# Optimization experiments

Hardware: AMD Instinct MI355X
Metric: run time of the kernel (lower is better)

## Reference

```python
import jax, jax.numpy as jnp
import numpy as np

D_MODEL = 1024
N_HEADS = 16
N_KV_HEADS = 4
HEAD_DIM = D_MODEL // N_HEADS  # 64
N_REP = N_HEADS // N_KV_HEADS  # 4
THETA = 10000.0
LOGIT_CAP = 30.0
EPS = 1e-6
SCALE = HEAD_DIM ** -0.5


def rmsnorm(x, w):
    return x * jax.lax.rsqrt(jnp.mean(x * x, axis=-1, keepdims=True) + EPS) * w


def rope_tables(seq_len, dtype):
    inv_freq = 1.0 / (THETA ** (jnp.arange(0, HEAD_DIM, 2, dtype=jnp.float32) / HEAD_DIM))
    t = jnp.arange(seq_len, dtype=jnp.float32)
    freqs = jnp.outer(t, inv_freq)                      # [S, hd/2]
    emb = jnp.concatenate([freqs, freqs], axis=-1)      # [S, hd]
    return jnp.cos(emb).astype(dtype), jnp.sin(emb).astype(dtype)


def rotate_half(x):
    x1, x2 = jnp.split(x, 2, axis=-1)
    return jnp.concatenate([-x2, x1], axis=-1)


def apply_rope(x, cos, sin):
    # x: [B, H, S, hd]; cos/sin: [S, hd] broadcast over (B, H)
    return x * cos + rotate_half(x) * sin


def setup_inputs() -> dict:
    key = jax.random.key(0)
    ks = jax.random.split(key, 7)
    B, S = 4, 2048
    w = 0.02
    return {
        "x": jax.random.normal(ks[0], (B, S, D_MODEL), dtype=jnp.float32),
        "Wq": jax.random.normal(ks[1], (N_HEADS * HEAD_DIM, D_MODEL), dtype=jnp.float32) * w,
        "Wk": jax.random.normal(ks[2], (N_KV_HEADS * HEAD_DIM, D_MODEL), dtype=jnp.float32) * w,
        "Wv": jax.random.normal(ks[3], (N_KV_HEADS * HEAD_DIM, D_MODEL), dtype=jnp.float32) * w,
        "Wo": jax.random.normal(ks[4], (D_MODEL, N_HEADS * HEAD_DIM), dtype=jnp.float32) * w,
        "q_norm_w": jnp.ones((HEAD_DIM,), dtype=jnp.float32),
        "k_norm_w": jnp.ones((HEAD_DIM,), dtype=jnp.float32),
    }


def reference(x, Wq, Wk, Wv, Wo, q_norm_w, k_norm_w):
    B, S, _ = x.shape
    # projections (nn.Linear: y = x @ W^T)
    q = (x @ Wq.T).reshape(B, S, N_HEADS, HEAD_DIM).transpose(0, 2, 1, 3)      # [B,H,S,d]
    k = (x @ Wk.T).reshape(B, S, N_KV_HEADS, HEAD_DIM).transpose(0, 2, 1, 3)   # [B,Hkv,S,d]
    v = (x @ Wv.T).reshape(B, S, N_KV_HEADS, HEAD_DIM).transpose(0, 2, 1, 3)
    # QK-RMSNorm
    q = rmsnorm(q, q_norm_w)
    k = rmsnorm(k, k_norm_w)
    # RoPE
    cos, sin = rope_tables(S, x.dtype)
    q = apply_rope(q, cos, sin)
    k = apply_rope(k, cos, sin)
    # GQA expand (repeat_interleave over head dim)
    k_exp = jnp.repeat(k, N_REP, axis=1)  # [B,H,S,d]
    v_exp = jnp.repeat(v, N_REP, axis=1)
    # soft-capped attention (training path)
    scores = jnp.einsum('bhqd,bhkd->bhqk', q, k_exp) * SCALE
    scores = LOGIT_CAP * jnp.tanh(scores / LOGIT_CAP)
    causal = jnp.triu(jnp.ones((S, S), dtype=bool), k=1)  # kv_len - seq_len + 1 = 1
    scores = jnp.where(causal, -jnp.inf, scores)
    attn = jax.nn.softmax(scores, axis=-1)
    out = jnp.einsum('bhqk,bhkd->bhqd', attn, v_exp)
    out = out.transpose(0, 2, 1, 3).reshape(B, S, N_HEADS * HEAD_DIM)
    return out @ Wo.T
```

## Files before the change

kernel.cpp:

```cpp
#include <hip/hip_runtime.h>
#include <hip/hip_bf16.h>
#include <math.h>
#include <stdint.h>

#define D_MODEL 1024
#define NHEADS  16
#define NKV     4
#define HD      64
#define SEQ     2048
#define BATCH   4
#define MTOK    (BATCH*SEQ)
#define NQKV    (D_MODEL + 2*NKV*HD)
#define ASCALE  0.125f
#define CAP     30.0f

using f32x4  = __attribute__((ext_vector_type(4))) float;
using bf16x8 = __attribute__((ext_vector_type(8))) short;

__device__ __forceinline__ unsigned short f2bf(float f) {
  union { float f; unsigned u; } v; v.f = f;
  unsigned u = v.u + 0x7fffu + ((v.u >> 16) & 1u);
  return (unsigned short)(u >> 16);
}
__device__ __forceinline__ unsigned short f2bf_hup(float f) {
  union { float f; unsigned u; } v; v.f = f;
  return (unsigned short)((v.u + 0x8000u) >> 16);
}
__device__ __forceinline__ float fexp2(float x) {
  return __builtin_amdgcn_exp2f(x);
}
__device__ __forceinline__ void async_copy16(void* lds, const void* g) {
  __builtin_amdgcn_global_load_lds(
      (const __attribute__((address_space(1))) unsigned int*)(uintptr_t)g,
      (__attribute__((address_space(3))) unsigned int*)(uintptr_t)lds, 16, 0, 0);
}

__global__ __launch_bounds__(256) void cvt_all(
    const float* __restrict__ x, const float* __restrict__ wq,
    const float* __restrict__ wk, const float* __restrict__ wv,
    const float* __restrict__ wo,
    unsigned short* __restrict__ xb, unsigned short* __restrict__ wqkv,
    unsigned short* __restrict__ wob) {
  const long i = (long)(blockIdx.x * 256 + threadIdx.x) * 4;
  const float* src; unsigned short* dst; long off;
  if (i < 8388608L)      { src = x;  dst = xb;             off = i; }
  else if (i < 9437184L) { src = wq; dst = wqkv;           off = i - 8388608L; }
  else if (i < 9699328L) { src = wk; dst = wqkv + 1048576; off = i - 9437184L; }
  else if (i < 9961472L) { src = wv; dst = wqkv + 1310720; off = i - 9699328L; }
  else                   { src = wo; dst = wob;            off = i - 9961472L; }
  float4 v = *(const float4*)(src + off);
  ushort4 o; o.x = f2bf(v.x); o.y = f2bf(v.y); o.z = f2bf(v.z); o.w = f2bf(v.w);
  *(ushort4*)(dst + off) = o;
}

__global__ __launch_bounds__(256) void gemm_qkv(
    const unsigned short* __restrict__ A, const unsigned short* __restrict__ B,
    const float* __restrict__ qw, const float* __restrict__ kw,
    unsigned short* __restrict__ Qn, unsigned short* __restrict__ Kn,
    unsigned short* __restrict__ Vt) {
  __shared__ __align__(16) unsigned short As[128 * 32];
  __shared__ __align__(16) unsigned short Bs[128 * 32];
  const int t = threadIdx.x;
  const int w = t >> 6, l = t & 63;
  const int mb = blockIdx.x, nb = blockIdx.y;
  const int wm = w & 1, wn = w >> 1;
  const int quad = l >> 4, ln = l & 15;
  const int K = D_MODEL;
  f32x4 acc[4][4] = {};
  const unsigned short* Ag = A + (size_t)(mb * 128 + w * 32) * K;
  const unsigned short* Bg = B + (size_t)(nb * 128 + w * 32) * K;
  char* Asw = (char*)As + w * 2048;
  char* Bsw = (char*)Bs + w * 2048;
  const int lrow = l >> 2, lcol = (l & 3) * 8;

  for (int kb = 0; kb < K; kb += 32) {
    async_copy16(Asw + l * 16,        Ag + (size_t)lrow * K + kb + lcol);
    async_copy16(Asw + 1024 + l * 16, Ag + (size_t)(16 + lrow) * K + kb + lcol);
    async_copy16(Bsw + l * 16,        Bg + (size_t)lrow * K + kb + lcol);
    async_copy16(Bsw + 1024 + l * 16, Bg + (size_t)(16 + lrow) * K + kb + lcol);
    __syncthreads();
    bf16x8 af[4], bfr[4];
#pragma unroll
    for (int mt = 0; mt < 4; ++mt)
      af[mt] = *(const bf16x8*)(As + (wm * 64 + mt * 16 + ln) * 32 + quad * 8);
#pragma unroll
    for (int nt = 0; nt < 4; ++nt)
      bfr[nt] = *(const bf16x8*)(Bs + (wn * 64 + nt * 16 + ln) * 32 + quad * 8);
#pragma unroll
    for (int mt = 0; mt < 4; ++mt)
#pragma unroll
      for (int nt = 0; nt < 4; ++nt)
        acc[mt][nt] = __builtin_amdgcn_mfma_f32_16x16x32_bf16(af[mt], bfr[nt], acc[mt][nt], 0, 0, 0);
    __syncthreads();
  }

  const int hs = nb * 2 + wn;
  const int bB = mb >> 4;
  const int sBase = ((mb & 15) * 128) + wm * 64;

  if (hs < 20) {
    const float* wgt = (hs < 16) ? qw : kw;
    float wv_[4];
#pragma unroll
    for (int nt = 0; nt < 4; ++nt) wv_[nt] = wgt[nt * 16 + ln];
    const float f0 = __expf(-(float)ln * 0.2878231366f);
    const float f1 = f0 * 0.01f;
    unsigned short* dst = (hs < 16)
        ? Qn + (size_t)(bB * 16 + hs) * SEQ * 64
        : Kn + (size_t)(bB * 4 + (hs - 16)) * SEQ * 64;
#pragma unroll
    for (int mt = 0; mt < 4; ++mt) {
#pragma unroll
      for (int r = 0; r < 4; ++r) {
        const int sTok = sBase + mt * 16 + quad * 4 + r;
        float ss = 0.f;
#pragma unroll
        for (int nt = 0; nt < 4; ++nt) ss = fmaf(acc[mt][nt][r], acc[mt][nt][r], ss);
        ss += __shfl_xor(ss, 1, 64); ss += __shfl_xor(ss, 2, 64);
        ss += __shfl_xor(ss, 4, 64); ss += __shfl_xor(ss, 8, 64);
        const float inv = rsqrtf(ss * (1.0f / 64.0f) + 1e-6f);
        float xn[4];
#pragma unroll
        for (int nt = 0; nt < 4; ++nt) xn[nt] = acc[mt][nt][r] * inv * wv_[nt];
        float sn0, cs0, sn1, cs1;
        __sincosf((float)sTok * f0, &sn0, &cs0);
        __sincosf((float)sTok * f1, &sn1, &cs1);
        const float o0 = xn[0] * cs0 - xn[2] * sn0;
        const float o1 = xn[1] * cs1 - xn[3] * sn1;
        const float o2 = xn[2] * cs0 + xn[0] * sn0;
        const float o3 = xn[3] * cs1 + xn[1] * sn1;
        const size_t ro = (size_t)sTok * 64 + ln;
        dst[ro]      = f2bf(o0);
        dst[ro + 16] = f2bf(o1);
        dst[ro + 32] = f2bf(o2);
        dst[ro + 48] = f2bf(o3);
      }
    }
  } else {
    unsigned short* dst = Vt + (size_t)(bB * 4 + (hs - 20)) * 64 * SEQ;
#pragma unroll
    for (int mt = 0; mt < 4; ++mt)
#pragma unroll
      for (int nt = 0; nt < 4; ++nt)
#pragma unroll
        for (int r = 0; r < 4; ++r) {
          const int sTok = sBase + mt * 16 + quad * 4 + r;
          dst[(size_t)(nt * 16 + ln) * SEQ + sTok] = f2bf(acc[mt][nt][r]);
        }
  }
}

__global__ __launch_bounds__(256) void gemm_bt_f32(
    const unsigned short* __restrict__ A, const unsigned short* __restrict__ B,
    float* __restrict__ C, int M, int N, int K) {
  __shared__ __align__(16) unsigned short As[128 * 32];
  __shared__ __align__(16) unsigned short Bs[128 * 32];
  const int t = threadIdx.x;
  const int w = t >> 6, l = t & 63;
  const int mb = blockIdx.x, nb = blockIdx.y;
  const int wm = w & 1, wn = w >> 1;
  f32x4 acc[4][4] = {};
  const unsigned short* Ag = A + (size_t)(mb * 128 + w * 32) * K;
  const unsigned short* Bg = B + (size_t)(nb * 128 + w * 32) * K;
  char* Asw = (char*)As + w * 2048;
  char* Bsw = (char*)Bs + w * 2048;
  const int lrow = l >> 2, lcol = (l & 3) * 8;

  for (int kb = 0; kb < K; kb += 32) {
    async_copy16(Asw + l * 16,        Ag + (size_t)lrow * K + kb + lcol);
    async_copy16(Asw + 1024 + l * 16, Ag + (size_t)(16 + lrow) * K + kb + lcol);
    async_copy16(Bsw + l * 16,        Bg + (size_t)lrow * K + kb + lcol);
    async_copy16(Bsw + 1024 + l * 16, Bg + (size_t)(16 + lrow) * K + kb + lcol);
    __syncthreads();
    bf16x8 af[4], bfr[4];
#pragma unroll
    for (int mt = 0; mt < 4; ++mt)
      af[mt] = *(const bf16x8*)(As + (wm * 64 + mt * 16 + (l & 15)) * 32 + (l >> 4) * 8);
#pragma unroll
    for (int nt = 0; nt < 4; ++nt)
      bfr[nt] = *(const bf16x8*)(Bs + (wn * 64 + nt * 16 + (l & 15)) * 32 + (l >> 4) * 8);
#pragma unroll
    for (int mt = 0; mt < 4; ++mt)
#pragma unroll
      for (int nt = 0; nt < 4; ++nt)
        acc[mt][nt] = __builtin_amdgcn_mfma_f32_16x16x32_bf16(af[mt], bfr[nt], acc[mt][nt], 0, 0, 0);
    __syncthreads();
  }
  const int row0 = mb * 128 + wm * 64, col0 = nb * 128 + wn * 64;
#pragma unroll
  for (int mt = 0; mt < 4; ++mt)
#pragma unroll
    for (int nt = 0; nt < 4; ++nt)
#pragma unroll
      for (int r = 0; r < 4; ++r) {
        int row = row0 + mt * 16 + (l >> 4) * 4 + r;
        int col = col0 + nt * 16 + (l & 15);
        C[(size_t)row * N + col] = acc[mt][nt][r];
      }
}

__global__ __launch_bounds__(256, 4) void attn(
    const unsigned short* __restrict__ Qn, const unsigned short* __restrict__ Kn,
    const unsigned short* __restrict__ Vtg, unsigned short* __restrict__ O) {
  __shared__ __align__(16) unsigned short Ks[4096];
  __shared__ __align__(16) unsigned short Vs[4096];
  __shared__ __align__(16) unsigned short Ps[8192];
  const int t = threadIdx.x, w = t >> 6, l = t & 63;
  const int quad = l >> 4, ln = l & 15;
  const int bid = blockIdx.x;
  const int jsl = bid & 3, krd = bid >> 8;
  const int qt = (krd & 1) ? (2 * jsl + (krd >> 1)) : (15 - 2 * jsl - (krd >> 1));
  const int bh = (bid >> 2) & 63;
  const int h = bh & 15, b = bh >> 4;
  const int q0 = qt * 128;
  const int wq0 = q0 + w * 32;
  const unsigned short* Qh = Qn + ((size_t)(b * 16 + h)) * SEQ * 64;
  const unsigned short* Kg = Kn + ((size_t)(b * 4 + (h >> 2))) * SEQ * 64;
  const unsigned short* Vg = Vtg + ((size_t)(b * 4 + (h >> 2))) * 64 * SEQ;
  const int lrow = l >> 2, lc = (l & 3) * 8;

  bf16x8 aq[2][2];
#pragma unroll
  for (int mt = 0; mt < 2; ++mt)
#pragma unroll
    for (int ks = 0; ks < 2; ++ks)
      aq[mt][ks] = *(const bf16x8*)(Qh + (size_t)(wq0 + mt * 16 + ln) * 64 + ks * 32 + quad * 8);
  f32x4 o_acc[2][4] = {};
  float l_part[2][4] = {};

  const float Cc = 0.18033688011112042f;
  const float B1 = -5.787037037e-6f;
  const float B2 = 4.0187757201e-11f;
  const float M2 = 11.541560327f;

  const int jmax = 2 * qt + 2;
  for (int jj = 0; jj < jmax; ++jj) {
    const int kv0 = jj * 64;
    __syncthreads();
#pragma unroll
    for (int i = 0; i < 2; ++i) {
      int s = w * 2 + i;
      int snt = s >> 1, sks = s & 1;
      async_copy16((char*)Ks + s * 1024,
                   Kg + (size_t)(kv0 + snt * 16 + lrow) * 64 + sks * 32 + lc);
      async_copy16((char*)Vs + s * 1024,
                   Vg + (size_t)(snt * 16 + lrow) * SEQ + kv0 + sks * 32 + lc);
    }
    __syncthreads();
    if (kv0 > wq0 + 31) continue;

    f32x4 sacc[2][4] = {};
#pragma unroll
    for (int nt = 0; nt < 4; ++nt)
#pragma unroll
      for (int ks = 0; ks < 2; ++ks) {
        bf16x8 bk = *(const bf16x8*)((char*)Ks + (nt * 2 + ks) * 1024 + ln * 64 + quad * 16);
        sacc[0][nt] = __builtin_amdgcn_mfma_f32_16x16x32_bf16(aq[0][ks], bk, sacc[0][nt], 0, 0, 0);
        sacc[1][nt] = __builtin_amdgcn_mfma_f32_16x16x32_bf16(aq[1][ks], bk, sacc[1][nt], 0, 0, 0);
      }

    const bool needMask = (kv0 + 63 > wq0);
#pragma unroll
    for (int mt = 0; mt < 2; ++mt)
#pragma unroll
      for (int nt = 0; nt < 4; ++nt) {
        const int col = nt * 16 + ln;
        const int base = w * 2048 + mt * 1024 + (col >> 5) * 512 +
                         ((((col >> 3) & 3) ^ quad) << 3) + (col & 7);
#pragma unroll
        for (int r = 0; r < 4; ++r) {
          float s = sacc[mt][nt][r];
          float s2 = s * s;
          float tt = fmaf(s2, B2, B1);
          tt = fmaf(s2, tt, 1.0f);
          float pr = fexp2(fmaf(s * Cc, tt, -M2));
          if (needMask && (kv0 + col) > (wq0 + mt * 16 + quad * 4 + r)) pr = 0.0f;
          l_part[mt][r] += pr;
          Ps[base + (quad * 4 + r) * 32] = f2bf_hup(pr);
        }
      }
    __builtin_amdgcn_s_waitcnt(0xc07f);

    bf16x8 ap[2][2];
#pragma unroll
    for (int mt = 0; mt < 2; ++mt)
#pragma unroll
      for (int ks = 0; ks < 2; ++ks)
        ap[mt][ks] = *(const bf16x8*)((char*)Ps + w * 4096 + mt * 2048 + ks * 1024 +
                                      ln * 64 + ((quad ^ (ln >> 2)) << 4));
#pragma unroll
    for (int nt = 0; nt < 4; ++nt)
#pragma unroll
      for (int ks = 0; ks < 2; ++ks) {
        bf16x8 bv = *(const bf16x8*)((char*)Vs + (nt * 2 + ks) * 1024 + ln * 64 + quad * 16);
        o_acc[0][nt] = __builtin_amdgcn_mfma_f32_16x16x32_bf16(ap[0][ks], bv, o_acc[0][nt], 0, 0, 0);
        o_acc[1][nt] = __builtin_amdgcn_mfma_f32_16x16x32_bf16(ap[1][ks], bv, o_acc[1][nt], 0, 0, 0);
      }
  }

  float invl[2][4];
#pragma unroll
  for (int mt = 0; mt < 2; ++mt)
#pragma unroll
    for (int r = 0; r < 4; ++r) {
      float s = l_part[mt][r];
      s += __shfl_xor(s, 1, 64); s += __shfl_xor(s, 2, 64);
      s += __shfl_xor(s, 4, 64); s += __shfl_xor(s, 8, 64);
      invl[mt][r] = __builtin_amdgcn_rcpf(s);
    }
#pragma unroll
  for (int mt = 0; mt < 2; ++mt)
#pragma unroll
    for (int nt = 0; nt < 4; ++nt)
#pragma unroll
      for (int r = 0; r < 4; ++r) {
        int qrow = wq0 + mt * 16 + quad * 4 + r;
        int col = h * 64 + nt * 16 + ln;
        O[((size_t)(b * SEQ + qrow)) * 1024 + col] = f2bf_hup(o_acc[mt][nt][r] * invl[mt][r]);
      }
}

extern "C" void kernel_launch(void* const* d_in, const int* in_sizes, int n_in,
                              void* d_out, int out_size, void* d_ws, size_t ws_size,
                              hipStream_t stream) {
  const float* x  = (const float*)d_in[0];
  const float* Wq = (const float*)d_in[1];
  const float* Wk = (const float*)d_in[2];
  const float* Wv = (const float*)d_in[3];
  const float* Wo = (const float*)d_in[4];
  const float* qw = (const float*)d_in[5];
  const float* kw = (const float*)d_in[6];
  float* out = (float*)d_out;

  char* ws = (char*)d_ws;
  unsigned short* xb   = (unsigned short*)(ws);
  unsigned short* wqkv = (unsigned short*)(ws + 16777216);
  unsigned short* wo   = (unsigned short*)(ws + 19922944);
  unsigned short* Qn   = (unsigned short*)(ws + 22020096);
  unsigned short* Kn   = (unsigned short*)(ws + 38797312);
  unsigned short* Vtg  = (unsigned short*)(ws + 42991616);
  unsigned short* Ob   = (unsigned short*)(ws + 47185920);

  cvt_all<<<10752, 256, 0, stream>>>(x, Wq, Wk, Wv, Wo, xb, wqkv, wo);
  gemm_qkv<<<dim3(MTOK / 128, NQKV / 128), 256, 0, stream>>>(xb, wqkv, qw, kw, Qn, Kn, Vtg);
  attn<<<1024, 256, 0, stream>>>(Qn, Kn, Vtg, Ob);
  gemm_bt_f32<<<dim3(MTOK / 128, 1024 / 128), 256, 0, stream>>>(Ob, wo, out, MTOK, 1024, 1024);
}
```

Before: 250.5 us.

## Pack softcap exponent math into float2 ops, drop cubic term, simplify tile order

Rewrites the per-score softcap and exponent computation on float2 vectors so the compiler can emit packed FP32 instructions (v_pk_fma/v_pk_mul), and drops the s^4 term of the tanh polynomial approximation. The row-sum accumulators become float2 pairs. Block-to-tile mapping also changes from an interleaved causal load-balancing order to a plain heavy-first order. Dropping the polynomial term loosens the tanh approximation for large scores, and the simpler schedule may balance causal work less evenly across CUs.

```diff
diff --git a/kernel.cpp b/kernel.cpp
--- a/kernel.cpp
+++ b/kernel.cpp
@@ -15,6 +15,7 @@
 #define CAP     30.0f
 
 using f32x4  = __attribute__((ext_vector_type(4))) float;
+using f32x2  = __attribute__((ext_vector_type(2))) float;
 using bf16x8 = __attribute__((ext_vector_type(8))) short;
 
 __device__ __forceinline__ unsigned short f2bf(float f) {
@@ -208,9 +209,8 @@
   const int t = threadIdx.x, w = t >> 6, l = t & 63;
   const int quad = l >> 4, ln = l & 15;
   const int bid = blockIdx.x;
-  const int jsl = bid & 3, krd = bid >> 8;
-  const int qt = (krd & 1) ? (2 * jsl + (krd >> 1)) : (15 - 2 * jsl - (krd >> 1));
-  const int bh = (bid >> 2) & 63;
+  const int qt = 15 - (bid >> 6);
+  const int bh = bid & 63;
   const int h = bh & 15, b = bh >> 4;
   const int q0 = qt * 128;
   const int wq0 = q0 + w * 32;
@@ -226,11 +226,10 @@
     for (int ks = 0; ks < 2; ++ks)
       aq[mt][ks] = *(const bf16x8*)(Qh + (size_t)(wq0 + mt * 16 + ln) * 64 + ks * 32 + quad * 8);
   f32x4 o_acc[2][4] = {};
-  float l_part[2][4] = {};
+  f32x2 lp[2][2] = {};
 
   const float Cc = 0.18033688011112042f;
   const float B1 = -5.787037037e-6f;
-  const float B2 = 4.0187757201e-11f;
   const float M2 = 11.541560327f;
 
   const int jmax = 2 * qt + 2;
@@ -268,15 +267,20 @@
         const int base = w * 2048 + mt * 1024 + (col >> 5) * 512 +
                          ((((col >> 3) & 3) ^ quad) << 3) + (col & 7);
 #pragma unroll
-        for (int r = 0; r < 4; ++r) {
-          float s = sacc[mt][nt][r];
-          float s2 = s * s;
-          float tt = fmaf(s2, B2, B1);
-          tt = fmaf(s2, tt, 1.0f);
-          float pr = fexp2(fmaf(s * Cc, tt, -M2));
-          if (needMask && (kv0 + col) > (wq0 + mt * 16 + quad * 4 + r)) pr = 0.0f;
-          l_part[mt][r] += pr;
-          Ps[base + (quad * 4 + r) * 32] = f2bf_hup(pr);
+        for (int rp = 0; rp < 2; ++rp) {
+          f32x2 s = { sacc[mt][nt][rp * 2], sacc[mt][nt][rp * 2 + 1] };
+          f32x2 s2 = s * s;
+          f32x2 tt = s2 * B1 + 1.0f;
+          f32x2 arg = (s * Cc) * tt - M2;
+          float pr0 = fexp2(arg.x), pr1 = fexp2(arg.y);
+          if (needMask) {
+            const int qrow = wq0 + mt * 16 + quad * 4 + rp * 2;
+            if ((kv0 + col) > qrow)     pr0 = 0.0f;
+            if ((kv0 + col) > qrow + 1) pr1 = 0.0f;
+          }
+          lp[mt][rp] += (f32x2){pr0, pr1};
+          Ps[base + (quad * 4 + rp * 2) * 32]     = f2bf_hup(pr0);
+          Ps[base + (quad * 4 + rp * 2 + 1) * 32] = f2bf_hup(pr1);
         }
       }
     __builtin_amdgcn_s_waitcnt(0xc07f);
@@ -303,7 +307,7 @@
   for (int mt = 0; mt < 2; ++mt)
 #pragma unroll
     for (int r = 0; r < 4; ++r) {
-      float s = l_part[mt][r];
+      float s = lp[mt][r >> 1][r & 1];
       s += __shfl_xor(s, 1, 64); s += __shfl_xor(s, 2, 64);
       s += __shfl_xor(s, 4, 64); s += __shfl_xor(s, 8, 64);
       invl[mt][r] = __builtin_amdgcn_rcpf(s);
```

Result: faster. 244.9 us (-2.3%).
